# Performance work log

Hardware: AMD Instinct MI355X
Metric: run time of the kernel (lower is better)

## Reference

```python
import jax, jax.numpy as jnp
import numpy as np

NMOD, NVEC, R, M, B = 4, 100000, 64, 512, 16384


def setup_inputs() -> dict:
    key = jax.random.key(0)
    ks = jax.random.split(key, 9)
    indices = jax.random.randint(ks[0], (B, NMOD), 0, NVEC, dtype=jnp.int32)
    # logit(U(0,1)) init for v_hat tables
    def logit_init(k):
        u = jax.random.uniform(k, (NVEC, R), dtype=jnp.float32, minval=1e-4, maxval=1.0 - 1e-4)
        return jnp.log(u) - jnp.log1p(-u)
    v0, v1, v2, v3 = (logit_init(ks[i]) for i in range(1, 5))
    S = jax.random.normal(ks[5], (M, NMOD * R), dtype=jnp.float32) / (2 * np.pi)
    b = jax.random.uniform(ks[6], (1, M), dtype=jnp.float32, minval=0.0, maxval=2 * np.pi)
    w_mu = jax.random.uniform(ks[7], (2 * M, 1), dtype=jnp.float32)
    return {"indices": indices, "v0": v0, "v1": v1, "v2": v2, "v3": v3,
            "S": S, "b": b, "w_mu": w_mu}


def _stick_break_gather(v_hat, idx):
    # Stick-breaking weights are computed row-wise (cumsum over axis=1),
    # so gathering rows first is mathematically identical to building the
    # full table and gathering (and far cheaper).
    vh = v_hat[idx]                       # [B, R]
    log_v = jax.nn.log_sigmoid(vh)
    log_vm = jax.nn.log_sigmoid(-vh)
    excl_cumsum = jnp.cumsum(log_vm, axis=1) - log_vm  # exclusive cumsum
    return jnp.exp(log_v + excl_cumsum)   # [B, R]


def reference(indices, v0, v1, v2, v3, S, b, w_mu):
    emb = jnp.concatenate([
        _stick_break_gather(v0, indices[:, 0]),
        _stick_break_gather(v1, indices[:, 1]),
        _stick_break_gather(v2, indices[:, 2]),
        _stick_break_gather(v3, indices[:, 3]),
    ], axis=1)                             # [B, 4R]
    phi_lin = emb @ S.T + b                # [B, M]
    phi = jnp.concatenate([jnp.cos(phi_lin), jnp.sin(phi_lin)], axis=1)  # [B, 2M]
    return jax.nn.sigmoid(phi @ w_mu)      # [B, 1]
```

## Files before the change

### kernel.cpp

```cpp
#include <hip/hip_runtime.h>
#include <math.h>

#define B_TOTAL 16384
#define RR 64
#define KK 256
#define MM 512
#define ROWS 16
#define NCH 8
#define NNI 8
#define ASTR 264
#define INV2PI 0.15915494309189535f

typedef __attribute__((ext_vector_type(8))) _Float16 half8;
typedef __attribute__((ext_vector_type(4))) float floatx4;

template<int CTRL, int RMASK>
static __device__ inline float dpp_mov1(float src) {
    int s = __builtin_bit_cast(int, src);
    int o = __builtin_bit_cast(int, 1.0f);
    int r = __builtin_amdgcn_update_dpp(o, s, CTRL, RMASK, 0xF, false);
    return __builtin_bit_cast(float, r);
}
template<int CTRL>
static __device__ inline float dpp_swap(float src) {
    int s = __builtin_bit_cast(int, src);
    int r = __builtin_amdgcn_update_dpp(s, s, CTRL, 0xF, 0xF, false);
    return __builtin_bit_cast(float, r);
}
static __device__ inline float red16(float x) {
    x += dpp_swap<0xB1>(x);
    x += dpp_swap<0x4E>(x);
    x += dpp_swap<0x141>(x);
    x += dpp_swap<0x140>(x);
    return x;
}

__global__ __launch_bounds__(256)
void conv_S(const float* __restrict__ S, _Float16* __restrict__ Bh)
{
    const int F = blockIdx.x * 256 + threadIdx.x;
    const int o = F >> 9;
    const int c = F & 511;
    const float* src = &S[c * KK + o * 8];
    float v[8];
    *reinterpret_cast<float4*>(&v[0]) = *reinterpret_cast<const float4*>(src);
    *reinterpret_cast<float4*>(&v[4]) = *reinterpret_cast<const float4*>(src + 4);
    half8 hv;
    #pragma unroll
    for (int j = 0; j < 8; ++j)
        hv[j] = (_Float16)(v[j] * INV2PI);
    *reinterpret_cast<half8*>(&Bh[F * 8]) = hv;
}

__global__ __launch_bounds__(256, 4)
void nest2_mfma(const int* __restrict__ indices,
                const float* __restrict__ v0, const float* __restrict__ v1,
                const float* __restrict__ v2, const float* __restrict__ v3,
                const _Float16* __restrict__ Bh,
                const float* __restrict__ bvec, const float* __restrict__ w_mu,
                float* __restrict__ out)
{
    __shared__ alignas(16) _Float16 Ah[ROWS * ASTR];
    __shared__ float red[4][ROWS];

    const int tid = threadIdx.x;
    const int rowBase = blockIdx.x * ROWS;
    const int wid  = __builtin_amdgcn_readfirstlane(tid >> 6);
    const int lane = tid & 63;
    const int l15  = lane & 15;
    const int lg   = lane >> 4;
    const int wcol0 = wid * 128;

    #define BOFF(ch, ni) ((((ch) * 4 + lg) * 512 + wcol0 + (ni) * 16 + l15) * 8)

    const int* ip = indices + rowBase * 4 + wid * 16;
    const float* vts[4] = {v0, v1, v2, v3};
    float vh[16];
    #pragma unroll
    for (int it = 0; it < 16; ++it) {
        const int mod = it & 3;
        vh[it] = vts[mod][ip[it] * RR + lane];
    }

    half8 b[NNI];
    #pragma unroll
    for (int ni = 0; ni < NNI; ++ni)
        b[ni] = *reinterpret_cast<const half8*>(&Bh[BOFF(0, ni)]);

    #pragma unroll
    for (int it = 0; it < 16; ++it) {
        const int p   = wid * 16 + it;
        const int row = p >> 2;
        const int mod = p & 3;
        const float t  = __expf(vh[it]);
        const float um = __builtin_amdgcn_rcpf(1.f + t);
        float pr = um;
        pr *= dpp_mov1<0x111, 0xF>(pr);
        pr *= dpp_mov1<0x112, 0xF>(pr);
        pr *= dpp_mov1<0x114, 0xF>(pr);
        pr *= dpp_mov1<0x118, 0xF>(pr);
        pr *= dpp_mov1<0x142, 0xA>(pr);
        pr *= dpp_mov1<0x143, 0xC>(pr);
        const float x = t * pr;
        Ah[row * ASTR + mod * RR + lane] = (_Float16)x;
    }
    __syncthreads();

    floatx4 acc[NNI];
    #pragma unroll
    for (int ni = 0; ni < NNI; ++ni)
        acc[ni] = (floatx4){0.f, 0.f, 0.f, 0.f};

    #pragma unroll
    for (int ch = 0; ch < NCH; ++ch) {
        const half8 ah = *reinterpret_cast<const half8*>(
            &Ah[l15 * ASTR + ch * 32 + lg * 8]);
        half8 bn[NNI];
        if (ch + 1 < NCH) {
            #pragma unroll
            for (int ni = 0; ni < NNI; ++ni)
                bn[ni] = *reinterpret_cast<const half8*>(&Bh[BOFF(ch + 1, ni)]);
        }
        __builtin_amdgcn_s_setprio(1);
        #pragma unroll
        for (int ni = 0; ni < NNI; ++ni)
            acc[ni] = __builtin_amdgcn_mfma_f32_16x16x32_f16(ah, b[ni], acc[ni], 0, 0, 0);
        __builtin_amdgcn_s_setprio(0);
        if (ch + 1 < NCH) {
            #pragma unroll
            for (int ni = 0; ni < NNI; ++ni)
                b[ni] = bn[ni];
        }
    }

    float rp[4] = {0.f, 0.f, 0.f, 0.f};
    #pragma unroll
    for (int ni = 0; ni < NNI; ++ni) {
        const int c = wcol0 + ni * 16 + l15;
        const float bb = bvec[c] * INV2PI;
        const float w1 = w_mu[c];
        const float w2 = w_mu[MM + c];
        #pragma unroll
        for (int r = 0; r < 4; ++r) {
            const float psi = acc[ni][r] + bb;
            const float sn = __builtin_amdgcn_sinf(psi);
            const float cs = __builtin_amdgcn_cosf(psi);
            rp[r] = fmaf(cs, w1, fmaf(sn, w2, rp[r]));
        }
    }

    #pragma unroll
    for (int r = 0; r < 4; ++r) {
        const float v = red16(rp[r]);
        if (l15 == 0) red[wid][lg * 4 + r] = v;
    }
    __syncthreads();

    if (tid < ROWS) {
        const float s = red[0][tid] + red[1][tid] + red[2][tid] + red[3][tid];
        out[rowBase + tid] = 1.f / (1.f + expf(-s));
    }
    #undef BOFF
}

extern "C" void kernel_launch(void* const* d_in, const int* in_sizes, int n_in,
                              void* d_out, int out_size, void* d_ws, size_t ws_size,
                              hipStream_t stream) {
    const int*   indices = (const int*)d_in[0];
    const float* v0 = (const float*)d_in[1];
    const float* v1 = (const float*)d_in[2];
    const float* v2 = (const float*)d_in[3];
    const float* v3 = (const float*)d_in[4];
    const float* S  = (const float*)d_in[5];
    const float* bb = (const float*)d_in[6];
    const float* w  = (const float*)d_in[7];
    float* out = (float*)d_out;

    _Float16* Bh = (_Float16*)d_ws;

    hipLaunchKernelGGL(conv_S, dim3(MM * KK / (256 * 8)), dim3(256), 0, stream,
                       S, Bh);
    hipLaunchKernelGGL(nest2_mfma, dim3(B_TOTAL / ROWS), dim3(256), 0, stream,
                       indices, v0, v1, v2, v3, Bh, bb, w, out);
}
```

Measured before the change: 22.11 us.

## Retile MFMA kernel to 32 rows per block with 8 waves and 2 M-subtiles

Each block now handles 32 rows with 512 threads. Each of the 8 waves covers 64 output columns and issues two 16-row MFMA subtiles, so each B fragment loaded from the fp16 S workspace is reused across twice as many rows. The goal is to halve per-row B-operand traffic through L2/L1. The bias and w_mu loads are also hoisted ahead of the stick-breaking phase so their latency overlaps it. In exchange the grid has half as many blocks, and the larger blocks bring more register pressure under the 512-thread launch bound.

```diff
diff --git a/kernel.cpp b/kernel.cpp
--- a/kernel.cpp
+++ b/kernel.cpp
@@ -5,9 +5,10 @@
 #define RR 64
 #define KK 256
 #define MM 512
-#define ROWS 16
+#define ROWS 32
 #define NCH 8
-#define NNI 8
+#define NNI 4
+#define MI 2
 #define ASTR 264
 #define INV2PI 0.15915494309189535f
 
@@ -52,7 +53,7 @@
     *reinterpret_cast<half8*>(&Bh[F * 8]) = hv;
 }
 
-__global__ __launch_bounds__(256, 4)
+__global__ __launch_bounds__(512, 4)
 void nest2_mfma(const int* __restrict__ indices,
                 const float* __restrict__ v0, const float* __restrict__ v1,
                 const float* __restrict__ v2, const float* __restrict__ v3,
@@ -61,7 +62,7 @@
                 float* __restrict__ out)
 {
     __shared__ alignas(16) _Float16 Ah[ROWS * ASTR];
-    __shared__ float red[4][ROWS];
+    __shared__ float red[8][ROWS];
 
     const int tid = threadIdx.x;
     const int rowBase = blockIdx.x * ROWS;
@@ -69,7 +70,7 @@
     const int lane = tid & 63;
     const int l15  = lane & 15;
     const int lg   = lane >> 4;
-    const int wcol0 = wid * 128;
+    const int wcol0 = wid * 64;
 
     #define BOFF(ch, ni) ((((ch) * 4 + lg) * 512 + wcol0 + (ni) * 16 + l15) * 8)
 
@@ -86,6 +87,14 @@
     #pragma unroll
     for (int ni = 0; ni < NNI; ++ni)
         b[ni] = *reinterpret_cast<const half8*>(&Bh[BOFF(0, ni)]);
+    float bbv[NNI], w1v[NNI], w2v[NNI];
+    #pragma unroll
+    for (int ni = 0; ni < NNI; ++ni) {
+        const int c = wcol0 + ni * 16 + l15;
+        bbv[ni] = bvec[c] * INV2PI;
+        w1v[ni] = w_mu[c];
+        w2v[ni] = w_mu[MM + c];
+    }
 
     #pragma unroll
     for (int it = 0; it < 16; ++it) {
@@ -106,15 +115,20 @@
     }
     __syncthreads();
 
-    floatx4 acc[NNI];
-    #pragma unroll
-    for (int ni = 0; ni < NNI; ++ni)
-        acc[ni] = (floatx4){0.f, 0.f, 0.f, 0.f};
+    floatx4 acc[MI][NNI];
+    #pragma unroll
+    for (int mi = 0; mi < MI; ++mi)
+        #pragma unroll
+        for (int ni = 0; ni < NNI; ++ni)
+            acc[mi][ni] = (floatx4){0.f, 0.f, 0.f, 0.f};
 
     #pragma unroll
     for (int ch = 0; ch < NCH; ++ch) {
-        const half8 ah = *reinterpret_cast<const half8*>(
-            &Ah[l15 * ASTR + ch * 32 + lg * 8]);
+        half8 ah[MI];
+        #pragma unroll
+        for (int mi = 0; mi < MI; ++mi)
+            ah[mi] = *reinterpret_cast<const half8*>(
+                &Ah[(mi * 16 + l15) * ASTR + ch * 32 + lg * 8]);
         half8 bn[NNI];
         if (ch + 1 < NCH) {
             #pragma unroll
@@ -124,7 +138,9 @@
         __builtin_amdgcn_s_setprio(1);
         #pragma unroll
         for (int ni = 0; ni < NNI; ++ni)
-            acc[ni] = __builtin_amdgcn_mfma_f32_16x16x32_f16(ah, b[ni], acc[ni], 0, 0, 0);
+            #pragma unroll
+            for (int mi = 0; mi < MI; ++mi)
+                acc[mi][ni] = __builtin_amdgcn_mfma_f32_16x16x32_f16(ah[mi], b[ni], acc[mi][ni], 0, 0, 0);
         __builtin_amdgcn_s_setprio(0);
         if (ch + 1 < NCH) {
             #pragma unroll
@@ -133,31 +149,38 @@
         }
     }
 
-    float rp[4] = {0.f, 0.f, 0.f, 0.f};
+    float rp[MI][4];
+    #pragma unroll
+    for (int mi = 0; mi < MI; ++mi)
+        #pragma unroll
+        for (int r = 0; r < 4; ++r) rp[mi][r] = 0.f;
+
     #pragma unroll
     for (int ni = 0; ni < NNI; ++ni) {
-        const int c = wcol0 + ni * 16 + l15;
-        const float bb = bvec[c] * INV2PI;
-        const float w1 = w_mu[c];
-        const float w2 = w_mu[MM + c];
+        #pragma unroll
+        for (int mi = 0; mi < MI; ++mi)
+            #pragma unroll
+            for (int r = 0; r < 4; ++r) {
+                const float psi = acc[mi][ni][r] + bbv[ni];
+                const float sn = __builtin_amdgcn_sinf(psi);
+                const float cs = __builtin_amdgcn_cosf(psi);
+                rp[mi][r] = fmaf(cs, w1v[ni], fmaf(sn, w2v[ni], rp[mi][r]));
+            }
+    }
+
+    #pragma unroll
+    for (int mi = 0; mi < MI; ++mi)
         #pragma unroll
         for (int r = 0; r < 4; ++r) {
-            const float psi = acc[ni][r] + bb;
-            const float sn = __builtin_amdgcn_sinf(psi);
-            const float cs = __builtin_amdgcn_cosf(psi);
-            rp[r] = fmaf(cs, w1, fmaf(sn, w2, rp[r]));
+            const float v = red16(rp[mi][r]);
+            if (l15 == 0) red[wid][mi * 16 + lg * 4 + r] = v;
         }
-    }
-
-    #pragma unroll
-    for (int r = 0; r < 4; ++r) {
-        const float v = red16(rp[r]);
-        if (l15 == 0) red[wid][lg * 4 + r] = v;
-    }
     __syncthreads();
 
     if (tid < ROWS) {
-        const float s = red[0][tid] + red[1][tid] + red[2][tid] + red[3][tid];
+        float s = 0.f;
+        #pragma unroll
+        for (int w = 0; w < 8; ++w) s += red[w][tid];
         out[rowBase + tid] = 1.f / (1.f + expf(-s));
     }
     #undef BOFF
@@ -180,6 +203,6 @@
 
     hipLaunchKernelGGL(conv_S, dim3(MM * KK / (256 * 8)), dim3(256), 0, stream,
                        S, Bh);
-    hipLaunchKernelGGL(nest2_mfma, dim3(B_TOTAL / ROWS), dim3(256), 0, stream,
+    hipLaunchKernelGGL(nest2_mfma, dim3(B_TOTAL / ROWS), dim3(512), 0, stream,
                        indices, v0, v1, v2, v3, Bh, bb, w, out);
 }
```

After: 18.94 us. 14.3% less time.
